# Optimization experiments

Hardware: AMD Instinct MI355X
Metric: run time of the kernel (lower is better)

## Reference

```python
import jax, jax.numpy as jnp
import numpy as np

B, N, C = 4, 2048, 1024
H = 16
D = C // H  # head_dim = 64

def setup_inputs() -> dict:
    key = jax.random.key(0)
    k1, k2, k3 = jax.random.split(key, 3)
    s = 1.0 / np.sqrt(C)
    x = jax.random.normal(k1, (B, N, C), dtype=jnp.float32)
    qkv_w = jax.random.normal(k2, (3 * C, C), dtype=jnp.float32) * s
    proj_w = jax.random.normal(k3, (C, C), dtype=jnp.float32) * s
    proj_b = jnp.zeros((C,), dtype=jnp.float32)
    return {"x": x, "qkv_w": qkv_w, "proj_w": proj_w, "proj_b": proj_b}

def reference(x, qkv_w, proj_w, proj_b):
    # qkv: torch Linear -> x @ W^T, no bias
    qkv = jnp.einsum('bnc,oc->bno', x, qkv_w)            # [B,N,3C]
    qkv = qkv.reshape(B, N, 3, H, D)
    q, k, v = qkv[:, :, 0], qkv[:, :, 1], qkv[:, :, 2]   # [B,N,H,D]
    scale = D ** -0.5
    scores = jnp.einsum('bqhd,bkhd->bhqk', q, k) * scale  # [B,H,N,N]
    causal = jnp.tril(jnp.ones((N, N), dtype=bool))
    scores = jnp.where(causal[None, None], scores, -jnp.inf)
    attn = jax.nn.softmax(scores, axis=-1)
    out = jnp.einsum('bhqk,bkhd->bqhd', attn, v).reshape(B, N, C)
    out = jnp.einsum('bnc,oc->bno', out, proj_w) + proj_b
    return out
```

## Files before the change

kernel.cpp:

```cpp
#include <hip/hip_runtime.h>
#include <math.h>

typedef __attribute__((ext_vector_type(8))) short short8;
typedef __attribute__((ext_vector_type(4))) short short4v;
typedef __attribute__((ext_vector_type(4))) float f32x4;
typedef __attribute__((ext_vector_type(4))) _Float16 half4v;

#define B_  4
#define N_  2048
#define C_  1024
#define H_  16
#define D_  64
#define TC3 3072

__device__ __forceinline__ short f2bf(float f) {
    unsigned u = __builtin_bit_cast(unsigned, f);
    u += 0x7fffu + ((u >> 16) & 1u);
    return (short)(u >> 16);
}

__device__ __forceinline__ half4v pack4h(float a, float b, float cc, float d) {
    auto lo = __builtin_amdgcn_cvt_pkrtz(a, b);
    auto hi = __builtin_amdgcn_cvt_pkrtz(cc, d);
    auto v4 = __builtin_shufflevector(lo, hi, 0, 1, 2, 3);
    return __builtin_bit_cast(half4v, v4);
}

__device__ __forceinline__ void gload16(const void* g, void* l) {
    __builtin_amdgcn_global_load_lds(
        (const __attribute__((address_space(1))) void*)g,
        (__attribute__((address_space(3))) void*)l, 16, 0, 0);
}

#define NX8  (B_ * N_ * C_ / 8)
#define NQ8  (TC3 * C_ / 8)
#define NP8  (C_ * C_ / 8)

__global__ __launch_bounds__(256) void cast_all(const float* __restrict__ x,
                                                const float* __restrict__ wq,
                                                const float* __restrict__ wp,
                                                short* __restrict__ xb,
                                                short* __restrict__ wqb,
                                                short* __restrict__ wpb) {
    int i = blockIdx.x * 256 + threadIdx.x;
    const float* src;
    short* dst;
    if (i < NX8) { src = x; dst = xb; }
    else if (i < NX8 + NQ8) { i -= NX8; src = wq; dst = wqb; }
    else { i -= NX8 + NQ8; src = wp; dst = wpb; }
    const float4 a = ((const float4*)src)[2 * i];
    const float4 b = ((const float4*)src)[2 * i + 1];
    short8 t;
    t[0] = f2bf(a.x); t[1] = f2bf(a.y); t[2] = f2bf(a.z); t[3] = f2bf(a.w);
    t[4] = f2bf(b.x); t[5] = f2bf(b.y); t[6] = f2bf(b.z); t[7] = f2bf(b.w);
    ((short8*)dst)[i] = t;
}

#define GK 64

template <int MODE>
__global__ __launch_bounds__(256) void gemm_bf16(const short* __restrict__ A,
                                                 const short* __restrict__ Bw,
                                                 const float* __restrict__ bias,
                                                 short* __restrict__ Qb,
                                                 short* __restrict__ Kb,
                                                 _Float16* __restrict__ Vtb,
                                                 float* __restrict__ Fout,
                                                 int M, int Nn, int K) {
    __shared__ short smem[2 * 128 * GK];
    short* As = smem;
    short* Bs = smem + 128 * GK;

    const int tid = threadIdx.x;
    const int w = tid >> 6;
    const int ln = tid & 63;
    const int wm = w >> 1;
    const int wn = w & 1;
    const int c = ln & 15;
    const int g = ln >> 4;
    const int c7 = c & 7;

    const int m0 = blockIdx.y * 128;
    const int n0 = blockIdx.x * 128;

    f32x4 acc[4][4];
#pragma unroll
    for (int m = 0; m < 4; ++m)
#pragma unroll
        for (int n = 0; n < 4; ++n) acc[m][n] = (f32x4){0.f, 0.f, 0.f, 0.f};

    const int srow = ln >> 3;
    const int sseg = (ln & 7) ^ srow;

    for (int k0 = 0; k0 < K; k0 += GK) {
#pragma unroll
        for (int j = 0; j < 4; ++j) {
            const int R0 = w * 32 + j * 8;
            const int row = R0 + srow;
            gload16(A + (size_t)(m0 + row) * K + k0 + sseg * 8, &As[R0 * GK]);
            gload16(Bw + (size_t)(n0 + row) * K + k0 + sseg * 8, &Bs[R0 * GK]);
        }
        asm volatile("s_waitcnt vmcnt(0)" ::: "memory");
        __syncthreads();

#pragma unroll
        for (int kh = 0; kh < 2; ++kh) {
            short8 aF[4], bF[4];
#pragma unroll
            for (int m = 0; m < 4; ++m)
                aF[m] = *(const short8*)&As[(wm * 64 + m * 16 + c) * GK +
                                            (((kh * 4 + g) ^ c7) * 8)];
#pragma unroll
            for (int n = 0; n < 4; ++n)
                bF[n] = *(const short8*)&Bs[(wn * 64 + n * 16 + c) * GK +
                                            (((kh * 4 + g) ^ c7) * 8)];
#pragma unroll
            for (int m = 0; m < 4; ++m)
#pragma unroll
                for (int n = 0; n < 4; ++n)
                    acc[m][n] = __builtin_amdgcn_mfma_f32_16x16x32_bf16(aF[m], bF[n], acc[m][n], 0, 0, 0);
        }
        __syncthreads();
    }

    if (MODE == 0) {
        const int mat = n0 >> 10;
        if (mat == 2) {
#pragma unroll
            for (int m = 0; m < 4; ++m) {
                const int row = m0 + wm * 64 + m * 16 + g * 4;
                const int b = row >> 11;
                const int nseq = row & 2047;
#pragma unroll
                for (int n = 0; n < 4; ++n) {
                    const int col = n0 + wn * 64 + n * 16 + c;
                    const int h = (col >> 6) & 15;
                    const int d = col & 63;
                    const half4v p = pack4h(acc[m][n][0], acc[m][n][1],
                                            acc[m][n][2], acc[m][n][3]);
                    *(half4v*)&Vtb[((size_t)(b * 16 + h) * 64 + d) * N_ + nseq] = p;
                }
            }
        } else {
            short* base = (mat == 0) ? Qb : Kb;
#pragma unroll
            for (int p = 0; p < 2; ++p) {
                __syncthreads();
                if (wn == p) {
#pragma unroll
                    for (int m = 0; m < 4; ++m)
#pragma unroll
                        for (int n = 0; n < 4; ++n)
#pragma unroll
                            for (int r = 0; r < 4; ++r)
                                smem[(wm * 64 + m * 16 + g * 4 + r) * 64 +
                                     (((n ^ g) * 16) + c)] = f2bf(acc[m][n][r]);
                }
                __syncthreads();
                const int row = tid >> 1;
                const int col0 = (tid & 1) * 32;
                const int gg = (row >> 2) & 3;
                const int grow = m0 + row;
                const int bb = grow >> 11, nseq = grow & 2047;
                const int h = ((n0 + p * 64) >> 6) & 15;
                short* dst = base + ((size_t)(bb * 16 + h) * N_ + nseq) * D_ + col0;
#pragma unroll
                for (int s16 = 0; s16 < 2; ++s16) {
                    const int Cb = col0 + s16 * 16;
                    const int ls_off = row * 64 + ((((Cb >> 4) ^ gg)) << 4);
                    *(short8*)(dst + s16 * 16) = *(const short8*)&smem[ls_off];
                    *(short8*)(dst + s16 * 16 + 8) = *(const short8*)&smem[ls_off + 8];
                }
            }
        }
    } else {
#pragma unroll
        for (int m = 0; m < 4; ++m) {
            const int row = m0 + wm * 64 + m * 16 + g * 4;
#pragma unroll
            for (int n = 0; n < 4; ++n) {
                const int col = n0 + wn * 64 + n * 16 + c;
                const float bv = bias[col];
#pragma unroll
                for (int r = 0; r < 4; ++r)
                    Fout[(size_t)(row + r) * Nn + col] = acc[m][n][r] + bv;
            }
        }
    }
}


__device__ __forceinline__ void stage_kv(const short* __restrict__ gK,
                                         const short* __restrict__ gV,
                                         short* KsB, short* VsB,
                                         int kt, int w, int lane) {
    const int sub = lane >> 3;
    const int sseg = (lane & 7) ^ sub;
#pragma unroll
    for (int j = 0; j < 2; ++j) {
        const int R0 = w * 16 + j * 8;
        const int row = R0 + sub;
        gload16(gK + (size_t)(kt * 64 + row) * D_ + sseg * 8, KsB + R0 * 64);
        gload16(gV + (size_t)row * N_ + kt * 64 + sseg * 8, VsB + R0 * 64);
    }
}

#define NITEMS 1024

__global__ __launch_bounds__(256, 4) void attn_fused(const short* __restrict__ Qb,
                                                     const short* __restrict__ Kb,
                                                     const _Float16* __restrict__ Vtb,
                                                     short* __restrict__ attnb,
                                                     unsigned int* __restrict__ counter) {
    __shared__ short Ks[2][64 * 64];
    __shared__ short Vts[2][64 * 64];
    __shared__ int s_item;

    const int tid = threadIdx.x;
    const int w = tid >> 6;
    const int lane = tid & 63;
    const int g = lane >> 4;
    const int c = lane & 15;
    const int swz = c & 7;

    for (;;) {
        __syncthreads();
        if (tid == 0) s_item = (int)atomicAdd(counter, 1u);
        __syncthreads();
        const int idx = s_item;
        if (idx >= NITEMS) return;

        const int qt = 15 - (idx >> 6);
        const int bh = idx & 63;
        const int b = bh >> 4, h = bh & 15;
        const int rowmin = qt * 128 + w * 32;
        const int nkt = 2 * qt + 2;

        const short* gK = Kb + (size_t)bh * N_ * D_;
        const short* gV = (const short*)(Vtb + (size_t)bh * D_ * N_);

        short8 aQ[2][2];
        {
            const short* qb0 = Qb + ((size_t)bh * N_ + rowmin) * D_;
#pragma unroll
            for (int m = 0; m < 2; ++m) {
                aQ[m][0] = *(const short8*)(qb0 + (m * 16 + c) * D_ + g * 8);
                aQ[m][1] = *(const short8*)(qb0 + (m * 16 + c) * D_ + 32 + g * 8);
            }
        }

        f32x4 Oacc[2][4];
#pragma unroll
        for (int m = 0; m < 2; ++m)
#pragma unroll
            for (int nt = 0; nt < 4; ++nt) Oacc[m][nt] = (f32x4){0.f, 0.f, 0.f, 0.f};
        float ls[2] = {0.f, 0.f};

        stage_kv(gK, gV, Ks[0], Vts[0], 0, w, lane);

        for (int kt = 0; kt < nkt; ++kt) {
            const short* KsB = Ks[kt & 1];
            const short* VsB = Vts[kt & 1];
            asm volatile("s_waitcnt vmcnt(0)" ::: "memory");
            __syncthreads();
            if (kt + 1 < nkt)
                stage_kv(gK, gV, Ks[(kt + 1) & 1], Vts[(kt + 1) & 1], kt + 1, w, lane);

            const int kvb = kt * 64;
            if (kvb > rowmin + 31) continue;
            const bool needmask = (kvb + 63) > rowmin;

            f32x4 S[2][4];
#pragma unroll
            for (int m = 0; m < 2; ++m)
#pragma unroll
                for (int n = 0; n < 4; ++n) S[m][n] = (f32x4){0.f, 0.f, 0.f, 0.f};
#pragma unroll
            for (int n = 0; n < 4; ++n) {
                const short* kr = KsB + (n * 16 + c) * 64;
                const short8 bk0 = *(const short8*)(kr + (g ^ swz) * 8);
                const short8 bk1 = *(const short8*)(kr + ((4 + g) ^ swz) * 8);
#pragma unroll
                for (int m = 0; m < 2; ++m) {
                    S[m][n] = __builtin_amdgcn_mfma_f32_16x16x32_bf16(bk0, aQ[m][0], S[m][n], 0, 0, 0);
                    S[m][n] = __builtin_amdgcn_mfma_f32_16x16x32_bf16(bk1, aQ[m][1], S[m][n], 0, 0, 0);
                }
            }

            half4v Pb[2][4];
#pragma unroll
            for (int m = 0; m < 2; ++m) {
                const int qrow = rowmin + m * 16 + c;
#pragma unroll
                for (int n = 0; n < 4; ++n) {
                    float p[4];
#pragma unroll
                    for (int r = 0; r < 4; ++r) {
                        float pv = __expf(fmaf(S[m][n][r], 0.125f, -4.0f));
                        if (needmask && (kvb + n * 16 + g * 4 + r) > qrow) pv = 0.f;
                        ls[m] += pv;
                        p[r] = pv;
                    }
                    Pb[m][n] = pack4h(p[0], p[1], p[2], p[3]);
                }
            }

#pragma unroll
            for (int n = 0; n < 4; ++n) {
#pragma unroll
                for (int nt = 0; nt < 4; ++nt) {
                    const int vrow = nt * 16 + c;
                    const int vseg = (n * 2 + (g >> 1)) ^ swz;
                    const half4v av = *(const half4v*)&VsB[vrow * 64 + vseg * 8 + (g & 1) * 4];
#pragma unroll
                    for (int m = 0; m < 2; ++m)
                        Oacc[m][nt] = __builtin_amdgcn_mfma_f32_16x16x16f16(av, Pb[m][n], Oacc[m][nt], 0, 0, 0);
                }
            }
        }

#pragma unroll
        for (int m = 0; m < 2; ++m) {
            ls[m] += __shfl_xor(ls[m], 16);
            ls[m] += __shfl_xor(ls[m], 32);
        }
#pragma unroll
        for (int m = 0; m < 2; ++m) {
            const float inv = 1.0f / ls[m];
            const int qrow = rowmin + m * 16 + c;
            short* dst = attnb + (size_t)(b * N_ + qrow) * C_ + h * D_;
#pragma unroll
            for (int nt = 0; nt < 4; ++nt) {
                short4v o;
#pragma unroll
                for (int r = 0; r < 4; ++r) o[r] = f2bf(Oacc[m][nt][r] * inv);
                *(short4v*)(dst + nt * 16 + g * 4) = o;
            }
        }
    }
}

extern "C" void kernel_launch(void* const* d_in, const int* in_sizes, int n_in,
                              void* d_out, int out_size, void* d_ws, size_t ws_size,
                              hipStream_t stream) {
    const float* x      = (const float*)d_in[0];
    const float* qkv_w  = (const float*)d_in[1];
    const float* proj_w = (const float*)d_in[2];
    const float* proj_b = (const float*)d_in[3];
    float* out = (float*)d_out;

    short* xb      = (short*)d_ws;
    short* qkv_wb  = xb + (size_t)B_ * N_ * C_;
    short* proj_wb = qkv_wb + (size_t)TC3 * C_;
    short* Qb      = proj_wb + (size_t)C_ * C_;
    short* Kb      = Qb + (size_t)B_ * H_ * N_ * D_;
    _Float16* Vtb  = (_Float16*)(Kb + (size_t)B_ * H_ * N_ * D_);
    short* attnb   = (short*)(Vtb + (size_t)B_ * H_ * N_ * D_);
    unsigned int* cnt = (unsigned int*)(attnb + (size_t)B_ * N_ * C_);

    const int M = B_ * N_;
    dim3 blk(256);

    hipMemsetAsync(cnt, 0, sizeof(unsigned int), stream);

    cast_all<<<dim3((NX8 + NQ8 + NP8) / 256), blk, 0, stream>>>(
        x, qkv_w, proj_w, xb, qkv_wb, proj_wb);

    gemm_bf16<0><<<dim3(TC3 / 128, M / 128), blk, 0, stream>>>(
        xb, qkv_wb, nullptr, Qb, Kb, Vtb, nullptr, M, TC3, C_);

    attn_fused<<<dim3(768), blk, 0, stream>>>(Qb, Kb, Vtb, attnb, cnt);

    gemm_bf16<1><<<dim3(C_ / 128, M / 128), blk, 0, stream>>>(
        attnb, proj_wb, proj_b, nullptr, nullptr, nullptr, out, M, C_, C_);
}
```

Baseline: 268.4 us.

## Replace atomic work queue with balanced paired query-tile blocks in attention

The persistent attention kernel with an atomic counter work queue is replaced by a static grid of 1024 blocks. Each block pairs a light query tile (p) with a heavy one (31-p) so every block does the same causal work, and each wave handles 16 rows from each tile. MFMA work is skipped at 16-column granularity past the diagonal, and s_setprio raises wave priority around the matrix sections. This removes the counter memset and atomics and balances load, but each wave now covers two scattered row groups and there are more blocks to schedule.

```diff
diff --git a/kernel.cpp b/kernel.cpp
--- a/kernel.cpp
+++ b/kernel.cpp
@@ -205,16 +205,12 @@
     }
 }
 
-#define NITEMS 1024
-
 __global__ __launch_bounds__(256, 4) void attn_fused(const short* __restrict__ Qb,
                                                      const short* __restrict__ Kb,
                                                      const _Float16* __restrict__ Vtb,
-                                                     short* __restrict__ attnb,
-                                                     unsigned int* __restrict__ counter) {
+                                                     short* __restrict__ attnb) {
     __shared__ short Ks[2][64 * 64];
     __shared__ short Vts[2][64 * 64];
-    __shared__ int s_item;
 
     const int tid = threadIdx.x;
     const int w = tid >> 6;
@@ -223,119 +219,122 @@
     const int c = lane & 15;
     const int swz = c & 7;
 
-    for (;;) {
+    const int bh = blockIdx.x >> 4;
+    const int p = blockIdx.x & 15;
+    const int b = bh >> 4, h = bh & 15;
+
+    const int uu[2] = {p, 31 - p};
+    const int rb[2] = {p * 64 + w * 16, (31 - p) * 64 + w * 16};
+    const int nkt = uu[1] + 1;
+
+    const short* gK = Kb + (size_t)bh * N_ * D_;
+    const short* gV = (const short*)(Vtb + (size_t)bh * D_ * N_);
+
+    short8 aQ[2][2];
+#pragma unroll
+    for (int m = 0; m < 2; ++m) {
+        const short* qb0 = Qb + ((size_t)bh * N_ + rb[m]) * D_;
+        aQ[m][0] = *(const short8*)(qb0 + c * D_ + g * 8);
+        aQ[m][1] = *(const short8*)(qb0 + c * D_ + 32 + g * 8);
+    }
+
+    f32x4 Oacc[2][4];
+#pragma unroll
+    for (int m = 0; m < 2; ++m)
+#pragma unroll
+        for (int nt = 0; nt < 4; ++nt) Oacc[m][nt] = (f32x4){0.f, 0.f, 0.f, 0.f};
+    float ls[2] = {0.f, 0.f};
+
+    stage_kv(gK, gV, Ks[0], Vts[0], 0, w, lane);
+
+    for (int kt = 0; kt < nkt; ++kt) {
+        const short* KsB = Ks[kt & 1];
+        const short* VsB = Vts[kt & 1];
+        asm volatile("s_waitcnt vmcnt(0)" ::: "memory");
         __syncthreads();
-        if (tid == 0) s_item = (int)atomicAdd(counter, 1u);
-        __syncthreads();
-        const int idx = s_item;
-        if (idx >= NITEMS) return;
-
-        const int qt = 15 - (idx >> 6);
-        const int bh = idx & 63;
-        const int b = bh >> 4, h = bh & 15;
-        const int rowmin = qt * 128 + w * 32;
-        const int nkt = 2 * qt + 2;
-
-        const short* gK = Kb + (size_t)bh * N_ * D_;
-        const short* gV = (const short*)(Vtb + (size_t)bh * D_ * N_);
-
-        short8 aQ[2][2];
-        {
-            const short* qb0 = Qb + ((size_t)bh * N_ + rowmin) * D_;
-#pragma unroll
-            for (int m = 0; m < 2; ++m) {
-                aQ[m][0] = *(const short8*)(qb0 + (m * 16 + c) * D_ + g * 8);
-                aQ[m][1] = *(const short8*)(qb0 + (m * 16 + c) * D_ + 32 + g * 8);
-            }
-        }
-
-        f32x4 Oacc[2][4];
-#pragma unroll
-        for (int m = 0; m < 2; ++m)
-#pragma unroll
-            for (int nt = 0; nt < 4; ++nt) Oacc[m][nt] = (f32x4){0.f, 0.f, 0.f, 0.f};
-        float ls[2] = {0.f, 0.f};
-
-        stage_kv(gK, gV, Ks[0], Vts[0], 0, w, lane);
-
-        for (int kt = 0; kt < nkt; ++kt) {
-            const short* KsB = Ks[kt & 1];
-            const short* VsB = Vts[kt & 1];
-            asm volatile("s_waitcnt vmcnt(0)" ::: "memory");
-            __syncthreads();
-            if (kt + 1 < nkt)
-                stage_kv(gK, gV, Ks[(kt + 1) & 1], Vts[(kt + 1) & 1], kt + 1, w, lane);
-
-            const int kvb = kt * 64;
-            if (kvb > rowmin + 31) continue;
-            const bool needmask = (kvb + 63) > rowmin;
-
-            f32x4 S[2][4];
-#pragma unroll
-            for (int m = 0; m < 2; ++m)
-#pragma unroll
-                for (int n = 0; n < 4; ++n) S[m][n] = (f32x4){0.f, 0.f, 0.f, 0.f};
+        if (kt + 1 < nkt)
+            stage_kv(gK, gV, Ks[(kt + 1) & 1], Vts[(kt + 1) & 1], kt + 1, w, lane);
+
+        const int kvb = kt * 64;
+
+        f32x4 S[2][4];
+        __builtin_amdgcn_s_setprio(1);
+#pragma unroll
+        for (int n = 0; n < 4; ++n) {
+            const bool a1 = (kvb + n * 16 <= rb[1] + 15);
+            const bool a0 = (kvb + n * 16 <= rb[0] + 15);
+            if (!a1) continue;
+            const short* kr = KsB + (n * 16 + c) * 64;
+            const short8 bk0 = *(const short8*)(kr + (g ^ swz) * 8);
+            const short8 bk1 = *(const short8*)(kr + ((4 + g) ^ swz) * 8);
+            f32x4 s1 = (f32x4){0.f, 0.f, 0.f, 0.f};
+            s1 = __builtin_amdgcn_mfma_f32_16x16x32_bf16(bk0, aQ[1][0], s1, 0, 0, 0);
+            s1 = __builtin_amdgcn_mfma_f32_16x16x32_bf16(bk1, aQ[1][1], s1, 0, 0, 0);
+            S[1][n] = s1;
+            if (a0) {
+                f32x4 s0 = (f32x4){0.f, 0.f, 0.f, 0.f};
+                s0 = __builtin_amdgcn_mfma_f32_16x16x32_bf16(bk0, aQ[0][0], s0, 0, 0, 0);
+                s0 = __builtin_amdgcn_mfma_f32_16x16x32_bf16(bk1, aQ[0][1], s0, 0, 0, 0);
+                S[0][n] = s0;
+            }
+        }
+        __builtin_amdgcn_s_setprio(0);
+
+        half4v Pb[2][4];
+#pragma unroll
+        for (int m = 0; m < 2; ++m) {
+            const int qrow = rb[m] + c;
+            const bool dm = (kt == uu[m]);
 #pragma unroll
             for (int n = 0; n < 4; ++n) {
-                const short* kr = KsB + (n * 16 + c) * 64;
-                const short8 bk0 = *(const short8*)(kr + (g ^ swz) * 8);
-                const short8 bk1 = *(const short8*)(kr + ((4 + g) ^ swz) * 8);
-#pragma unroll
-                for (int m = 0; m < 2; ++m) {
-                    S[m][n] = __builtin_amdgcn_mfma_f32_16x16x32_bf16(bk0, aQ[m][0], S[m][n], 0, 0, 0);
-                    S[m][n] = __builtin_amdgcn_mfma_f32_16x16x32_bf16(bk1, aQ[m][1], S[m][n], 0, 0, 0);
+                if (kvb + n * 16 > rb[m] + 15) continue;
+                float pv0[4];
+#pragma unroll
+                for (int r = 0; r < 4; ++r) {
+                    float pv = __expf(fmaf(S[m][n][r], 0.125f, -4.0f));
+                    if (dm && (kvb + n * 16 + g * 4 + r) > qrow) pv = 0.f;
+                    ls[m] += pv;
+                    pv0[r] = pv;
                 }
-            }
-
-            half4v Pb[2][4];
-#pragma unroll
-            for (int m = 0; m < 2; ++m) {
-                const int qrow = rowmin + m * 16 + c;
-#pragma unroll
-                for (int n = 0; n < 4; ++n) {
-                    float p[4];
-#pragma unroll
-                    for (int r = 0; r < 4; ++r) {
-                        float pv = __expf(fmaf(S[m][n][r], 0.125f, -4.0f));
-                        if (needmask && (kvb + n * 16 + g * 4 + r) > qrow) pv = 0.f;
-                        ls[m] += pv;
-                        p[r] = pv;
-                    }
-                    Pb[m][n] = pack4h(p[0], p[1], p[2], p[3]);
-                }
-            }
-
-#pragma unroll
-            for (int n = 0; n < 4; ++n) {
-#pragma unroll
-                for (int nt = 0; nt < 4; ++nt) {
-                    const int vrow = nt * 16 + c;
-                    const int vseg = (n * 2 + (g >> 1)) ^ swz;
-                    const half4v av = *(const half4v*)&VsB[vrow * 64 + vseg * 8 + (g & 1) * 4];
-#pragma unroll
-                    for (int m = 0; m < 2; ++m)
-                        Oacc[m][nt] = __builtin_amdgcn_mfma_f32_16x16x16f16(av, Pb[m][n], Oacc[m][nt], 0, 0, 0);
-                }
-            }
-        }
-
-#pragma unroll
-        for (int m = 0; m < 2; ++m) {
-            ls[m] += __shfl_xor(ls[m], 16);
-            ls[m] += __shfl_xor(ls[m], 32);
-        }
-#pragma unroll
-        for (int m = 0; m < 2; ++m) {
-            const float inv = 1.0f / ls[m];
-            const int qrow = rowmin + m * 16 + c;
-            short* dst = attnb + (size_t)(b * N_ + qrow) * C_ + h * D_;
+                Pb[m][n] = pack4h(pv0[0], pv0[1], pv0[2], pv0[3]);
+            }
+        }
+
+        __builtin_amdgcn_s_setprio(1);
+#pragma unroll
+        for (int n = 0; n < 4; ++n) {
+            const bool a1 = (kvb + n * 16 <= rb[1] + 15);
+            const bool a0 = (kvb + n * 16 <= rb[0] + 15);
+            if (!a1) continue;
 #pragma unroll
             for (int nt = 0; nt < 4; ++nt) {
-                short4v o;
-#pragma unroll
-                for (int r = 0; r < 4; ++r) o[r] = f2bf(Oacc[m][nt][r] * inv);
-                *(short4v*)(dst + nt * 16 + g * 4) = o;
-            }
+                const int vrow = nt * 16 + c;
+                const int vseg = (n * 2 + (g >> 1)) ^ swz;
+                const half4v av = *(const half4v*)&VsB[vrow * 64 + vseg * 8 + (g & 1) * 4];
+                Oacc[1][nt] = __builtin_amdgcn_mfma_f32_16x16x16f16(av, Pb[1][n], Oacc[1][nt], 0, 0, 0);
+                if (a0)
+                    Oacc[0][nt] = __builtin_amdgcn_mfma_f32_16x16x16f16(av, Pb[0][n], Oacc[0][nt], 0, 0, 0);
+            }
+        }
+        __builtin_amdgcn_s_setprio(0);
+    }
+
+#pragma unroll
+    for (int m = 0; m < 2; ++m) {
+        ls[m] += __shfl_xor(ls[m], 16);
+        ls[m] += __shfl_xor(ls[m], 32);
+    }
+#pragma unroll
+    for (int m = 0; m < 2; ++m) {
+        const float inv = 1.0f / ls[m];
+        const int qrow = rb[m] + c;
+        short* dst = attnb + (size_t)(b * N_ + qrow) * C_ + h * D_;
+#pragma unroll
+        for (int nt = 0; nt < 4; ++nt) {
+            short4v o;
+#pragma unroll
+            for (int r = 0; r < 4; ++r) o[r] = f2bf(Oacc[m][nt][r] * inv);
+            *(short4v*)(dst + nt * 16 + g * 4) = o;
         }
     }
 }
@@ -356,20 +355,17 @@
     short* Kb      = Qb + (size_t)B_ * H_ * N_ * D_;
     _Float16* Vtb  = (_Float16*)(Kb + (size_t)B_ * H_ * N_ * D_);
     short* attnb   = (short*)(Vtb + (size_t)B_ * H_ * N_ * D_);
-    unsigned int* cnt = (unsigned int*)(attnb + (size_t)B_ * N_ * C_);
 
     const int M = B_ * N_;
     dim3 blk(256);
 
-    hipMemsetAsync(cnt, 0, sizeof(unsigned int), stream);
-
     cast_all<<<dim3((NX8 + NQ8 + NP8) / 256), blk, 0, stream>>>(
         x, qkv_w, proj_w, xb, qkv_wb, proj_wb);
 
     gemm_bf16<0><<<dim3(TC3 / 128, M / 128), blk, 0, stream>>>(
         xb, qkv_wb, nullptr, Qb, Kb, Vtb, nullptr, M, TC3, C_);
 
-    attn_fused<<<dim3(768), blk, 0, stream>>>(Qb, Kb, Vtb, attnb, cnt);
+    attn_fused<<<dim3(1024), blk, 0, stream>>>(Qb, Kb, Vtb, attnb);
 
     gemm_bf16<1><<<dim3(C_ / 128, M / 128), blk, 0, stream>>>(
         attnb, proj_wb, proj_b, nullptr, nullptr, nullptr, out, M, C_, C_);
```

Result: slower. 296.2 us (+10.4%).

## Software-pipeline QK^T one tile ahead with split K/V staging

Applied to the files above, without the earlier changes.

Splits K and V staging so that K is prefetched two tiles ahead and V one tile ahead. The QK^T MFMAs for the next tile are issued before the softmax and PV work of the current tile, using ping-pong S register arrays. The aim is to overlap the exp/softmax VALU work with matrix-core work and to hide LDS latency. The cost is higher register pressure from holding two S arrays, which may hurt occupancy at launch_bounds(256,4). If nkt is odd, the second step in each pair must still behave correctly.

```diff
diff --git a/kernel.cpp b/kernel.cpp
--- a/kernel.cpp
+++ b/kernel.cpp
@@ -190,10 +190,8 @@
 }
 
 
-__device__ __forceinline__ void stage_kv(const short* __restrict__ gK,
-                                         const short* __restrict__ gV,
-                                         short* KsB, short* VsB,
-                                         int kt, int w, int lane) {
+__device__ __forceinline__ void stage_k(const short* __restrict__ gK,
+                                        short* KsB, int kt, int w, int lane) {
     const int sub = lane >> 3;
     const int sseg = (lane & 7) ^ sub;
 #pragma unroll
@@ -201,6 +199,17 @@
         const int R0 = w * 16 + j * 8;
         const int row = R0 + sub;
         gload16(gK + (size_t)(kt * 64 + row) * D_ + sseg * 8, KsB + R0 * 64);
+    }
+}
+
+__device__ __forceinline__ void stage_v(const short* __restrict__ gV,
+                                        short* VsB, int kt, int w, int lane) {
+    const int sub = lane >> 3;
+    const int sseg = (lane & 7) ^ sub;
+#pragma unroll
+    for (int j = 0; j < 2; ++j) {
+        const int R0 = w * 16 + j * 8;
+        const int row = R0 + sub;
         gload16(gV + (size_t)row * N_ + kt * 64 + sseg * 8, VsB + R0 * 64);
     }
 }
@@ -256,67 +265,89 @@
             for (int nt = 0; nt < 4; ++nt) Oacc[m][nt] = (f32x4){0.f, 0.f, 0.f, 0.f};
         float ls[2] = {0.f, 0.f};
 
-        stage_kv(gK, gV, Ks[0], Vts[0], 0, w, lane);
-
-        for (int kt = 0; kt < nkt; ++kt) {
-            const short* KsB = Ks[kt & 1];
-            const short* VsB = Vts[kt & 1];
+        f32x4 Sa[2][4], Sb[2][4];
+
+        stage_k(gK, Ks[0], 0, w, lane);
+        stage_v(gV, Vts[0], 0, w, lane);
+        stage_k(gK, Ks[1], 1, w, lane);
+        asm volatile("s_waitcnt vmcnt(4)" ::: "memory");
+        __syncthreads();
+#pragma unroll
+        for (int n = 0; n < 4; ++n) {
+            const short* kr = Ks[0] + (n * 16 + c) * 64;
+            const short8 bk0 = *(const short8*)(kr + (g ^ swz) * 8);
+            const short8 bk1 = *(const short8*)(kr + ((4 + g) ^ swz) * 8);
+#pragma unroll
+            for (int m = 0; m < 2; ++m) {
+                f32x4 s = (f32x4){0.f, 0.f, 0.f, 0.f};
+                s = __builtin_amdgcn_mfma_f32_16x16x32_bf16(bk0, aQ[m][0], s, 0, 0, 0);
+                s = __builtin_amdgcn_mfma_f32_16x16x32_bf16(bk1, aQ[m][1], s, 0, 0, 0);
+                Sa[m][n] = s;
+            }
+        }
+
+        auto step = [&](int KT, f32x4 (&SC)[2][4], f32x4 (&SN)[2][4], int Pc) {
             asm volatile("s_waitcnt vmcnt(0)" ::: "memory");
             __syncthreads();
-            if (kt + 1 < nkt)
-                stage_kv(gK, gV, Ks[(kt + 1) & 1], Vts[(kt + 1) & 1], kt + 1, w, lane);
-
-            const int kvb = kt * 64;
-            if (kvb > rowmin + 31) continue;
-            const bool needmask = (kvb + 63) > rowmin;
-
-            f32x4 S[2][4];
-#pragma unroll
-            for (int m = 0; m < 2; ++m)
-#pragma unroll
-                for (int n = 0; n < 4; ++n) S[m][n] = (f32x4){0.f, 0.f, 0.f, 0.f};
-#pragma unroll
-            for (int n = 0; n < 4; ++n) {
-                const short* kr = KsB + (n * 16 + c) * 64;
-                const short8 bk0 = *(const short8*)(kr + (g ^ swz) * 8);
-                const short8 bk1 = *(const short8*)(kr + ((4 + g) ^ swz) * 8);
+            if (KT + 2 < nkt) stage_k(gK, Ks[Pc], KT + 2, w, lane);
+            if (KT + 1 < nkt) stage_v(gV, Vts[Pc ^ 1], KT + 1, w, lane);
+
+            if ((KT + 1 < nkt) && ((KT + 1) * 64 <= rowmin + 31)) {
+                const short* kb = Ks[Pc ^ 1];
+#pragma unroll
+                for (int n = 0; n < 4; ++n) {
+                    const short* kr = kb + (n * 16 + c) * 64;
+                    const short8 bk0 = *(const short8*)(kr + (g ^ swz) * 8);
+                    const short8 bk1 = *(const short8*)(kr + ((4 + g) ^ swz) * 8);
+#pragma unroll
+                    for (int m = 0; m < 2; ++m) {
+                        f32x4 s = (f32x4){0.f, 0.f, 0.f, 0.f};
+                        s = __builtin_amdgcn_mfma_f32_16x16x32_bf16(bk0, aQ[m][0], s, 0, 0, 0);
+                        s = __builtin_amdgcn_mfma_f32_16x16x32_bf16(bk1, aQ[m][1], s, 0, 0, 0);
+                        SN[m][n] = s;
+                    }
+                }
+            }
+
+            if (KT * 64 <= rowmin + 31) {
+                const int kvb = KT * 64;
+                const bool needmask = (kvb + 63) > rowmin;
+                half4v Pb[2][4];
 #pragma unroll
                 for (int m = 0; m < 2; ++m) {
-                    S[m][n] = __builtin_amdgcn_mfma_f32_16x16x32_bf16(bk0, aQ[m][0], S[m][n], 0, 0, 0);
-                    S[m][n] = __builtin_amdgcn_mfma_f32_16x16x32_bf16(bk1, aQ[m][1], S[m][n], 0, 0, 0);
-                }
-            }
-
-            half4v Pb[2][4];
-#pragma unroll
-            for (int m = 0; m < 2; ++m) {
-                const int qrow = rowmin + m * 16 + c;
+                    const int qrow = rowmin + m * 16 + c;
+#pragma unroll
+                    for (int n = 0; n < 4; ++n) {
+                        float p[4];
+#pragma unroll
+                        for (int r = 0; r < 4; ++r) {
+                            float pv = __expf(fmaf(SC[m][n][r], 0.125f, -4.0f));
+                            if (needmask && (kvb + n * 16 + g * 4 + r) > qrow) pv = 0.f;
+                            ls[m] += pv;
+                            p[r] = pv;
+                        }
+                        Pb[m][n] = pack4h(p[0], p[1], p[2], p[3]);
+                    }
+                }
+                const short* VsB = Vts[Pc];
 #pragma unroll
                 for (int n = 0; n < 4; ++n) {
-                    float p[4];
-#pragma unroll
-                    for (int r = 0; r < 4; ++r) {
-                        float pv = __expf(fmaf(S[m][n][r], 0.125f, -4.0f));
-                        if (needmask && (kvb + n * 16 + g * 4 + r) > qrow) pv = 0.f;
-                        ls[m] += pv;
-                        p[r] = pv;
+#pragma unroll
+                    for (int nt = 0; nt < 4; ++nt) {
+                        const int vrow = nt * 16 + c;
+                        const int vseg = (n * 2 + (g >> 1)) ^ swz;
+                        const half4v av = *(const half4v*)&VsB[vrow * 64 + vseg * 8 + (g & 1) * 4];
+#pragma unroll
+                        for (int m = 0; m < 2; ++m)
+                            Oacc[m][nt] = __builtin_amdgcn_mfma_f32_16x16x16f16(av, Pb[m][n], Oacc[m][nt], 0, 0, 0);
                     }
-                    Pb[m][n] = pack4h(p[0], p[1], p[2], p[3]);
-                }
-            }
-
-#pragma unroll
-            for (int n = 0; n < 4; ++n) {
-#pragma unroll
-                for (int nt = 0; nt < 4; ++nt) {
-                    const int vrow = nt * 16 + c;
-                    const int vseg = (n * 2 + (g >> 1)) ^ swz;
-                    const half4v av = *(const half4v*)&VsB[vrow * 64 + vseg * 8 + (g & 1) * 4];
-#pragma unroll
-                    for (int m = 0; m < 2; ++m)
-                        Oacc[m][nt] = __builtin_amdgcn_mfma_f32_16x16x16f16(av, Pb[m][n], Oacc[m][nt], 0, 0, 0);
-                }
-            }
+                }
+            }
+        };
+
+        for (int kt = 0; kt < nkt; kt += 2) {
+            step(kt, Sa, Sb, 0);
+            step(kt + 1, Sb, Sa, 1);
         }
 
 #pragma unroll
```

Result: slower. 360.1 us (+34.2%).
